# Performance work log

Measured on AMD Instinct MI355X. Metric: run time of the kernel, lower is better.

## Reference

```python
import jax, jax.numpy as jnp
import numpy as np

B, NQ, NC, D, H, HD, FF, RB = 2, 512, 2048, 768, 12, 64, 3072, 64
EPS = 1e-5


def setup_inputs() -> dict:
    key = jax.random.key(0)
    ks = jax.random.split(key, 20)
    def n(k, shape, s=0.02):
        return jax.random.normal(k, shape, jnp.float32) * s
    return dict(
        query_state=n(ks[0], (B, NQ, D), 1.0),
        context_k=n(ks[1], (B, NC, D), 1.0),
        context_v=n(ks[2], (B, NC, D), 1.0),
        query_coords=jax.random.uniform(ks[3], (B, NQ, 2), jnp.float32),
        context_coords=jax.random.uniform(ks[4], (B, NC, 2), jnp.float32),
        sn_g=jnp.ones(D), sn_b=jnp.zeros(D),
        wqkv=n(ks[5], (D, 3 * D)), bqkv=jnp.zeros(3 * D),
        wo_s=n(ks[6], (D, D)), bo_s=jnp.zeros(D),
        cn_g=jnp.ones(D), cn_b=jnp.zeros(D),
        wq=n(ks[7], (D, D)), bq=jnp.zeros(D),
        wk=n(ks[8], (D, D)), bk=jnp.zeros(D),
        wv=n(ks[9], (D, D)), bv=jnp.zeros(D),
        wo_c=n(ks[10], (D, D)), bo_c=jnp.zeros(D),
        rb_w1=n(ks[11], (2, RB), 0.5), rb_b1=jnp.zeros(RB),
        rb_w2=n(ks[12], (RB, H), 0.5), rb_b2=jnp.zeros(H),
        fn_g=jnp.ones(D), fn_b=jnp.zeros(D),
        fw1=n(ks[13], (D, FF)), fb1=jnp.zeros(FF),
        fw2=n(ks[14], (FF, D)), fb2=jnp.zeros(D),
    )


def _ln(x, g, b):
    m = x.mean(-1, keepdims=True)
    v = ((x - m) ** 2).mean(-1, keepdims=True)
    return (x - m) / jnp.sqrt(v + EPS) * g + b


def _heads(x):
    # (B, N, D) -> (B, H, N, HD)
    return x.reshape(x.shape[0], x.shape[1], H, HD).transpose(0, 2, 1, 3)


def reference(query_state, context_k, context_v, query_coords, context_coords,
              sn_g, sn_b, wqkv, bqkv, wo_s, bo_s,
              cn_g, cn_b, wq, bq, wk, bk, wv, bv, wo_c, bo_c,
              rb_w1, rb_b1, rb_w2, rb_b2,
              fn_g, fn_b, fw1, fb1, fw2, fb2):
    scale = HD ** -0.5
    x = query_state

    # ---- pre-norm self-attention (nn.MultiheadAttention equivalent) ----
    qn = _ln(x, sn_g, sn_b)
    qkv = qn @ wqkv + bqkv                      # (B, NQ, 3D)
    q, k, v = jnp.split(qkv, 3, axis=-1)
    q, k, v = _heads(q), _heads(k), _heads(v)   # (B, H, NQ, HD)
    a = jax.nn.softmax(jnp.einsum('bhqd,bhkd->bhqk', q, k) * scale, axis=-1)
    o = jnp.einsum('bhqk,bhkd->bhqd', a, v).transpose(0, 2, 1, 3).reshape(B, NQ, D)
    x = x + o @ wo_s + bo_s

    # ---- relative coordinate bias: MLP(delta) -> (B, H, NQ, NC) ----
    delta = query_coords[:, :, None, :] - context_coords[:, None, :, :]  # (B, NQ, NC, 2)
    bias = jax.nn.gelu(delta @ rb_w1 + rb_b1, approximate=False) @ rb_w2 + rb_b2
    bias = bias.transpose(0, 3, 1, 2)           # (B, H, NQ, NC)

    # ---- pre-norm cross-attention with bias ----
    qn = _ln(x, cn_g, cn_b)
    q = _heads(qn @ wq + bq)                    # (B, H, NQ, HD)
    k = _heads(context_k @ wk + bk)             # (B, H, NC, HD)
    v = _heads(context_v @ wv + bv)
    logits = jnp.einsum('bhqd,bhkd->bhqk', q, k) * scale + bias
    a = jax.nn.softmax(logits, axis=-1)
    o = jnp.einsum('bhqk,bhkd->bhqd', a, v).transpose(0, 2, 1, 3).reshape(B, NQ, D)
    x = x + o @ wo_c + bo_c

    # ---- pre-norm FFN ----
    h = jax.nn.gelu(_ln(x, fn_g, fn_b) @ fw1 + fb1, approximate=False)
    x = x + h @ fw2 + fb2
    return x
```

## Files before the change

kernel.cpp:

```cpp
#include <hip/hip_runtime.h>

#define B_ 2
#define NQ_ 512
#define NC_ 2048
#define D_ 768
#define H_ 12
#define HD_ 64
#define FF_ 3072
#define RB_ 64

typedef unsigned short u16;
typedef __attribute__((ext_vector_type(4))) unsigned short u16x4;
typedef __attribute__((ext_vector_type(8))) short short8;
typedef __attribute__((ext_vector_type(4))) float f32x4;
typedef __attribute__((ext_vector_type(2))) float f32x2;

#define SCL2 0.18033688f

__device__ __forceinline__ float bf2f(u16 u) {
    unsigned int i = ((unsigned int)u) << 16;
    float f; __builtin_memcpy(&f, &i, 4); return f;
}
__device__ __forceinline__ u16 f2bf(float f) {
    unsigned int i; __builtin_memcpy(&i, &f, 4);
    unsigned int r = i + 0x7FFFu + ((i >> 16) & 1u);
    return (u16)(r >> 16);
}
__device__ __forceinline__ float gelu_f(float x) {
    return 0.5f * x * (1.f + erff(x * 0.70710678118654752f));
}
__device__ __forceinline__ float wsum(float v) {
    v += __shfl_xor(v, 32); v += __shfl_xor(v, 16); v += __shfl_xor(v, 8);
    v += __shfl_xor(v, 4);  v += __shfl_xor(v, 2);  v += __shfl_xor(v, 1);
    return v;
}
__device__ __forceinline__ void gload_lds16(const void* g, void* l) {
    __builtin_amdgcn_global_load_lds((const __attribute__((address_space(1))) void*)g,
                                     (__attribute__((address_space(3))) void*)l, 16, 0, 0);
}

__device__ __forceinline__ void wtrans_body(const float* __restrict__ in, u16* __restrict__ out,
                                            int K, int N, int bx, int by, int tid) {
    __shared__ float t[32][33];
    int n0 = bx * 32, k0 = by * 32;
    int tx = tid & 31, ty = tid >> 5;
#pragma unroll
    for (int r = 0; r < 4; ++r)
        t[ty + r * 8][tx] = in[(long)(k0 + ty + r * 8) * N + n0 + tx];
    __syncthreads();
#pragma unroll
    for (int r = 0; r < 4; ++r)
        out[(long)(n0 + ty + r * 8) * K + k0 + tx] = f2bf(t[tx][ty + r * 8]);
}

__global__ __launch_bounds__(256) void wtrans(const float* __restrict__ in, u16* __restrict__ out,
                                              int K, int N) {
    wtrans_body(in, out, K, N, blockIdx.x, blockIdx.y, threadIdx.x);
}

__global__ __launch_bounds__(256) void wtrans5(const float* i0, const float* i1, const float* i2,
                                               const float* i3, const float* i4,
                                               u16* o0, u16* o1, u16* o2, u16* o3, u16* o4) {
    const float* in; u16* out;
    switch (blockIdx.z) {
        case 0: in = i0; out = o0; break;
        case 1: in = i1; out = o1; break;
        case 2: in = i2; out = o2; break;
        case 3: in = i3; out = o3; break;
        default: in = i4; out = o4; break;
    }
    wtrans_body(in, out, 768, 768, blockIdx.x, blockIdx.y, threadIdx.x);
}

__global__ __launch_bounds__(256) void cvtk2(const float* __restrict__ inA, u16* __restrict__ outA,
                                             const float* __restrict__ inB, u16* __restrict__ outB, int n4) {
    int i = blockIdx.x * 256 + threadIdx.x;
    const float* in = blockIdx.y ? inB : inA;
    u16* out = blockIdx.y ? outB : outA;
    if (i < n4) {
        float4 v = ((const float4*)in)[i];
        u16x4 o; o.x = f2bf(v.x); o.y = f2bf(v.y); o.z = f2bf(v.z); o.w = f2bf(v.w);
        ((u16x4*)out)[i] = o;
    }
}

__global__ __launch_bounds__(256) void catbias(const float* __restrict__ a, const float* __restrict__ b,
                                               float* __restrict__ o) {
    int i = blockIdx.x * 256 + threadIdx.x;
    if (i < 768) o[i] = a[i];
    else if (i < 1536) o[i] = b[i - 768];
}

__global__ __launch_bounds__(256) void ln_k(const float* __restrict__ x, const float* __restrict__ g,
                                            const float* __restrict__ bta, u16* __restrict__ out) {
    int row = blockIdx.x, t = threadIdx.x;
    const float* xr = x + (long)row * D_;
    float a0 = xr[t], a1 = xr[t + 256], a2 = xr[t + 512];
    float s = a0 + a1 + a2, s2 = a0 * a0 + a1 * a1 + a2 * a2;
    s = wsum(s); s2 = wsum(s2);
    __shared__ float rb[8];
    int lane = t & 63, wid = t >> 6;
    if (!lane) { rb[wid] = s; rb[wid + 4] = s2; }
    __syncthreads();
    float S = rb[0] + rb[1] + rb[2] + rb[3];
    float S2 = rb[4] + rb[5] + rb[6] + rb[7];
    float mean = S * (1.f / D_);
    float var = S2 * (1.f / D_) - mean * mean;
    float rstd = rsqrtf(var + 1e-5f);
    u16* orow = out + (long)row * D_;
    orow[t]       = f2bf((a0 - mean) * rstd * g[t]       + bta[t]);
    orow[t + 256] = f2bf((a1 - mean) * rstd * g[t + 256] + bta[t + 256]);
    orow[t + 512] = f2bf((a2 - mean) * rstd * g[t + 512] + bta[t + 512]);
}

__global__ __launch_bounds__(256) void bias_mlp7(
    const float* __restrict__ qcoord, const float* __restrict__ ccoord,
    const float* __restrict__ w1, const float* __restrict__ b1,
    const float* __restrict__ w2, const float* __restrict__ b2,
    u16* __restrict__ out) {
    __shared__ float s1[192];
    __shared__ float sw2[RB_ * H_];
    __shared__ float2 sc[256];
    __shared__ u16 sb[12 * 264];
    int tid = threadIdx.x;
    int b = blockIdx.z, q0 = blockIdx.y * 4, c0 = blockIdx.x * 256;
    if (tid < 64) { s1[tid] = w1[tid]; s1[64 + tid] = w1[64 + tid]; s1[128 + tid] = b1[tid]; }
    for (int i = tid; i < RB_ * H_; i += 256) sw2[i] = w2[i];
    sc[tid] = ((const float2*)ccoord)[b * NC_ + c0 + tid];
    __syncthreads();
    int lane = tid & 63, wid = tid >> 6;
    int h = lane & 15, g4 = lane >> 4;
    int j0 = g4 * 8;
    f32x2 wx[8], wy[8], bb[8];
#pragma unroll
    for (int p = 0; p < 4; ++p) {
        wx[p]     = (f32x2){s1[j0 + 2 * p],       s1[j0 + 2 * p + 1]};
        wy[p]     = (f32x2){s1[64 + j0 + 2 * p],  s1[64 + j0 + 2 * p + 1]};
        bb[p]     = (f32x2){s1[128 + j0 + 2 * p], s1[128 + j0 + 2 * p + 1]};
        wx[4 + p] = (f32x2){s1[32 + j0 + 2 * p],  s1[32 + j0 + 2 * p + 1]};
        wy[4 + p] = (f32x2){s1[96 + j0 + 2 * p],  s1[96 + j0 + 2 * p + 1]};
        bb[4 + p] = (f32x2){s1[160 + j0 + 2 * p], s1[160 + j0 + 2 * p + 1]};
    }
    short8 vb0, vb1;
#pragma unroll
    for (int u = 0; u < 8; ++u) {
        vb0[u] = (h < 12) ? (short)f2bf(sw2[(j0 + u) * H_ + h]) : (short)0;
        vb1[u] = (h < 12) ? (short)f2bf(sw2[(32 + j0 + u) * H_ + h]) : (short)0;
    }
    float qx[4], qy[4];
#pragma unroll
    for (int qq = 0; qq < 4; ++qq) {
        qx[qq] = qcoord[(b * NQ_ + q0 + qq) * 2];
        qy[qq] = qcoord[(b * NQ_ + q0 + qq) * 2 + 1];
    }
    float b2v = (h < 12) ? b2[h] : 0.f;
#pragma unroll 1
    for (int qq = 0; qq < 4; ++qq) {
        if (qq) __syncthreads();
#pragma unroll
        for (int it = 0; it < 4; ++it) {
            int ci = wid * 64 + it * 16 + h;
            float2 cc = sc[ci];
            float dx = qx[qq] - cc.x, dy = qy[qq] - cc.y;
            unsigned int pk[8];
#pragma unroll
            for (int p = 0; p < 8; ++p) {
                f32x2 pre = dx * wx[p] + bb[p];
                pre = dy * wy[p] + pre;
                f32x2 xc = __builtin_elementwise_min(
                               __builtin_elementwise_max(pre, (f32x2)(-3.0f)), (f32x2)(3.0f));
                f32x2 u = xc * xc;
                f32x2 v = u * 2.3813e-5f + (-6.8939e-4f);
                v = v * u + 0.0086261f;
                v = v * u + (-0.064949f);
                v = v * u + 0.39837f;
                f32x2 phi = xc * v + 0.5f;
                f32x2 g = pre * phi;
                pk[p] = __builtin_amdgcn_perm(__builtin_bit_cast(unsigned int, g.y),
                                              __builtin_bit_cast(unsigned int, g.x), 0x07060302u);
            }
            uint4 d0 = {pk[0], pk[1], pk[2], pk[3]};
            uint4 d1 = {pk[4], pk[5], pk[6], pk[7]};
            short8 a0 = __builtin_bit_cast(short8, d0);
            short8 a1 = __builtin_bit_cast(short8, d1);
            f32x4 acc = {};
            acc = __builtin_amdgcn_mfma_f32_16x16x32_bf16(a0, vb0, acc, 0, 0, 0);
            acc = __builtin_amdgcn_mfma_f32_16x16x32_bf16(a1, vb1, acc, 0, 0, 0);
            if (h < 12) {
#pragma unroll
                for (int r = 0; r < 4; ++r) {
                    int loc = wid * 64 + it * 16 + g4 * 4 + r;
                    sb[h * 264 + loc] = f2bf((acc[r] + b2v) * 1.4426950f);
                }
            }
        }
        __syncthreads();
        for (int i = tid; i < 12 * 128; i += 256) {
            int row = i >> 7, cp = (i & 127) * 2;
            unsigned int pv = *(const unsigned int*)(sb + row * 264 + cp);
            *(unsigned int*)(out + (((long)(b * H_ + row) * NQ_ + q0 + qq) * NC_ + c0 + cp)) = pv;
        }
    }
}

__global__ __launch_bounds__(256) void vtrans(const u16* __restrict__ in, u16* __restrict__ out,
                                              int NCt, int ldin, int bdiv, long sIb, long sIh) {
    __shared__ u16 t[32][33];
    int z = blockIdx.z, zb = z / bdiv, zh = z % bdiv;
    const u16* ib = in + zb * sIb + zh * sIh;
    int c0 = blockIdx.x * 32, d0 = blockIdx.y * 32;
    int tx = threadIdx.x & 31, ty = threadIdx.x >> 5;
#pragma unroll
    for (int r = 0; r < 4; ++r)
        t[ty + r * 8][tx] = ib[(long)(c0 + ty + r * 8) * ldin + d0 + tx];
    __syncthreads();
#pragma unroll
    for (int r = 0; r < 4; ++r)
        out[(long)z * 64 * NCt + (long)(d0 + ty + r * 8) * NCt + c0 + tx] = t[tx][ty + r * 8];
}

template <int NCT, bool HASBIAS>
__global__ __launch_bounds__(64) void fattn(
    const u16* __restrict__ Qb, const u16* __restrict__ Kb, const u16* __restrict__ Vtb,
    const u16* __restrict__ Bias, u16* __restrict__ Ob, int ldq, int ldk) {
    __shared__ u16 kl[2][128 * 64];
    __shared__ u16 vl[64 * 128];
    __shared__ u16 pl[16 * 128];
    const int lane = threadIdx.x;
    const int h16 = lane & 15, g4 = lane >> 4;
    const int hh = blockIdx.y, b = blockIdx.z, q0 = blockIdx.x * 16;
    const u16* Qrow = Qb + (long)(b * NQ_ + q0 + h16) * ldq + hh * 64;
    short8 qf0 = *(const short8*)(Qrow + g4 * 8);
    short8 qf1 = *(const short8*)(Qrow + 32 + g4 * 8);
    const u16* Kbase = Kb + (long)b * NCT * ldk + hh * 64;
    const u16* Vtbase = Vtb + (long)(b * H_ + hh) * 64 * NCT;

    auto stageK = [&](int buf, int c0) {
#pragma unroll
        for (int i = 0; i < 16; ++i) {
            int ch = i * 64 + lane;
            int row = ch >> 3, col2 = (ch & 7) * 16;
            int scol2 = col2 ^ ((row & 7) << 4);
            gload_lds16(Kbase + (long)(c0 + row) * ldk + (scol2 >> 1), &kl[buf][ch * 8]);
        }
    };
    auto stageV = [&](int c0) {
#pragma unroll
        for (int i = 0; i < 16; ++i) {
            int ch = i * 64 + lane;
            int row = ch >> 4, col2 = (ch & 15) * 16;
            int scol2 = col2 ^ ((row & 15) << 4);
            gload_lds16(Vtbase + (long)row * NCT + c0 + (scol2 >> 1), &vl[ch * 8]);
        }
    };

    float m0[4] = {-1e30f, -1e30f, -1e30f, -1e30f};
    float l0[4] = {0.f, 0.f, 0.f, 0.f};
    f32x4 oacc[4] = {};
    constexpr int T = NCT / 128;
    stageK(0, 0);
    for (int t = 0; t < T; ++t) {
        const int c0 = t * 128, cur = t & 1;
        asm volatile("s_waitcnt lgkmcnt(0)" ::: "memory");
        stageV(c0);
        if (t + 1 < T) stageK(cur ^ 1, c0 + 128);
        if (t + 1 < T) asm volatile("s_waitcnt vmcnt(32)" ::: "memory");
        else           asm volatile("s_waitcnt vmcnt(16)" ::: "memory");
        f32x4 sacc[8] = {};
        const u16* klc = kl[cur];
        __builtin_amdgcn_s_setprio(1);
#pragma unroll
        for (int n = 0; n < 8; ++n) {
            int row = n * 16 + h16, swz = (row & 7) << 4;
#pragma unroll
            for (int ks = 0; ks < 2; ++ks) {
                short8 kf = *(const short8*)((const char*)klc + row * 128 + ((ks * 64 + g4 * 16) ^ swz));
                sacc[n] = __builtin_amdgcn_mfma_f32_16x16x32_bf16(ks ? qf1 : qf0, kf, sacc[n], 0, 0, 0);
            }
        }
        __builtin_amdgcn_s_setprio(0);
        if (t + 1 < T) asm volatile("s_waitcnt vmcnt(16)" ::: "memory");
        else           asm volatile("s_waitcnt vmcnt(0)" ::: "memory");
        float cr[4];
#pragma unroll
        for (int r = 0; r < 4; ++r) {
            float mx = -1e30f;
#pragma unroll
            for (int n = 0; n < 8; ++n) {
                float s = sacc[n][r] * SCL2;
                sacc[n][r] = s; mx = fmaxf(mx, s);
            }
            mx = fmaxf(mx, __shfl_xor(mx, 1)); mx = fmaxf(mx, __shfl_xor(mx, 2));
            mx = fmaxf(mx, __shfl_xor(mx, 4)); mx = fmaxf(mx, __shfl_xor(mx, 8));
            float mn = fmaxf(m0[r], mx);
            cr[r] = __builtin_amdgcn_exp2f(m0[r] - mn); m0[r] = mn;
            float sum = 0.f;
#pragma unroll
            for (int n = 0; n < 8; ++n) {
                float p = __builtin_amdgcn_exp2f(sacc[n][r] - mn); sacc[n][r] = p; sum += p;
            }
            sum += __shfl_xor(sum, 1); sum += __shfl_xor(sum, 2);
            sum += __shfl_xor(sum, 4); sum += __shfl_xor(sum, 8);
            l0[r] = l0[r] * cr[r] + sum;
        }
#pragma unroll
        for (int n = 0; n < 8; ++n)
#pragma unroll
            for (int r = 0; r < 4; ++r) {
                int q = g4 * 4 + r, c = n * 16 + h16;
                *(u16*)((char*)pl + q * 256 + ((c * 2) ^ (q << 4))) =
                    (u16)(__builtin_bit_cast(unsigned int, sacc[n][r]) >> 16);
            }
#pragma unroll
        for (int d = 0; d < 4; ++d) {
            f32x4 o = oacc[d];
            o[0] *= cr[0]; o[1] *= cr[1]; o[2] *= cr[2]; o[3] *= cr[3];
            oacc[d] = o;
        }
        short8 pf[4];
#pragma unroll
        for (int ks = 0; ks < 4; ++ks)
            pf[ks] = *(const short8*)((const char*)pl + h16 * 256 + ((ks * 64 + g4 * 16) ^ (h16 << 4)));
        __builtin_amdgcn_s_setprio(1);
#pragma unroll
        for (int d = 0; d < 4; ++d) {
            int row = d * 16 + h16, swzv = (row & 15) << 4;
#pragma unroll
            for (int ks = 0; ks < 4; ++ks) {
                short8 vf = *(const short8*)((const char*)vl + row * 256 + ((ks * 64 + g4 * 16) ^ swzv));
                oacc[d] = __builtin_amdgcn_mfma_f32_16x16x32_bf16(pf[ks], vf, oacc[d], 0, 0, 0);
            }
        }
        __builtin_amdgcn_s_setprio(0);
    }
    float inv[4];
#pragma unroll
    for (int r = 0; r < 4; ++r) inv[r] = 1.f / l0[r];
    u16* Orow = Ob + (long)(b * NQ_ + q0) * D_ + hh * 64;
#pragma unroll
    for (int d = 0; d < 4; ++d)
#pragma unroll
        for (int r = 0; r < 4; ++r)
            Orow[(long)(g4 * 4 + r) * D_ + d * 16 + h16] = f2bf(oacc[d][r] * inv[r]);
}

template <int T, int S>
__global__ __launch_bounds__(256) void fattn4(
    const u16* __restrict__ Qb, const u16* __restrict__ Kb, const u16* __restrict__ Vtb,
    const u16* __restrict__ Bias, float* __restrict__ Part,
    int ldq, int ldk, int ldv, int NCT) {
    __shared__ u16 kl[2][64 * 64];
    __shared__ u16 vl[64 * 64];
    __shared__ u16 bl[4][16 * 64];
    __shared__ u16 pl[4][16 * 64];
    const int tid = threadIdx.x, lane = tid & 63, wid = tid >> 6;
    const int h16 = lane & 15, g4 = lane >> 4;
    const int qb = blockIdx.x, hh = blockIdx.y;
    const int b = blockIdx.z / S, s = blockIdx.z % S;
    const int q0w = qb * 64 + wid * 16;
    const int cb = s * (T * 64);
    const u16* Qrow = Qb + (long)(b * NQ_ + q0w + h16) * ldq + hh * 64;
    short8 qf0 = *(const short8*)(Qrow + g4 * 8);
    short8 qf1 = *(const short8*)(Qrow + 32 + g4 * 8);
    const u16* Kbase = Kb + (long)b * NCT * ldk + hh * 64;
    const u16* Vtbase = Vtb + (long)(b * H_ + hh) * 64 * ldv;
    const u16* Bbase = Bias + ((long)(b * H_ + hh) * NQ_ + q0w) * NCT;
    u16* mypl = pl[wid];
    const u16* mybl = bl[wid];

    auto stageK = [&](int buf, int c0) {
#pragma unroll
        for (int i = 0; i < 2; ++i) {
            int ch = wid * 128 + i * 64 + lane;
            int row = ch >> 3, col2 = (ch & 7) * 16;
            int scol2 = col2 ^ ((row & 7) << 4);
            gload_lds16(Kbase + (long)(c0 + row) * ldk + (scol2 >> 1), &kl[buf][ch * 8]);
        }
    };
    auto stageV = [&](int c0) {
#pragma unroll
        for (int i = 0; i < 2; ++i) {
            int ch = wid * 128 + i * 64 + lane;
            int row = ch >> 3, col2 = (ch & 7) * 16;
            int scol2 = col2 ^ ((row & 7) << 4);
            gload_lds16(Vtbase + (long)row * ldv + c0 + (scol2 >> 1), &vl[ch * 8]);
        }
    };
    auto stageB = [&](int c0) {
#pragma unroll
        for (int i = 0; i < 2; ++i) {
            int ch = i * 64 + lane;
            int row = ch >> 3, c16 = ch & 7;
            int sc16 = c16 ^ (row & 7);
            gload_lds16(Bbase + (long)row * NCT + c0 + sc16 * 8, &bl[wid][ch * 8]);
        }
    };

    float m0[4] = {-1e30f, -1e30f, -1e30f, -1e30f};
    float l0[4] = {0.f, 0.f, 0.f, 0.f};
    f32x4 oacc[4] = {};
    stageK(0, cb);
    for (int t = 0; t < T; ++t) {
        const int c0 = cb + t * 64, cur = t & 1;
        if (t > 0) {
            asm volatile("s_waitcnt lgkmcnt(0)" ::: "memory");
            __builtin_amdgcn_sched_barrier(0);
            __builtin_amdgcn_s_barrier();
        }
        stageV(c0);
        stageB(c0);
        if (t + 1 < T) stageK(cur ^ 1, c0 + 64);
        if (t + 1 < T) asm volatile("s_waitcnt vmcnt(6)" ::: "memory");
        else           asm volatile("s_waitcnt vmcnt(4)" ::: "memory");
        __builtin_amdgcn_s_barrier();
        f32x4 sacc[4] = {};
        const u16* klc = kl[cur];
        __builtin_amdgcn_s_setprio(1);
#pragma unroll
        for (int n = 0; n < 4; ++n) {
            int row = n * 16 + h16, swz = (row & 7) << 4;
#pragma unroll
            for (int ks = 0; ks < 2; ++ks) {
                short8 kf = *(const short8*)((const char*)klc + row * 128 + ((ks * 64 + g4 * 16) ^ swz));
                sacc[n] = __builtin_amdgcn_mfma_f32_16x16x32_bf16(ks ? qf1 : qf0, kf, sacc[n], 0, 0, 0);
            }
        }
        __builtin_amdgcn_s_setprio(0);
        if (t + 1 < T) asm volatile("s_waitcnt vmcnt(2)" ::: "memory");
        else           asm volatile("s_waitcnt vmcnt(0)" ::: "memory");
        __builtin_amdgcn_s_barrier();
        float cr[4];
#pragma unroll
        for (int r = 0; r < 4; ++r) {
            int q = g4 * 4 + r;
            float mx = -1e30f;
#pragma unroll
            for (int n = 0; n < 4; ++n) {
                float bvv = bf2f(*(const u16*)((const char*)mybl + q * 128 +
                                 (((n * 16 + h16) * 2) ^ ((q & 7) << 4))));
                float sv = sacc[n][r] * SCL2 + bvv;
                sacc[n][r] = sv; mx = fmaxf(mx, sv);
            }
            mx = fmaxf(mx, __shfl_xor(mx, 1)); mx = fmaxf(mx, __shfl_xor(mx, 2));
            mx = fmaxf(mx, __shfl_xor(mx, 4)); mx = fmaxf(mx, __shfl_xor(mx, 8));
            float mn = fmaxf(m0[r], mx);
            cr[r] = __builtin_amdgcn_exp2f(m0[r] - mn); m0[r] = mn;
            float sum = 0.f;
#pragma unroll
            for (int n = 0; n < 4; ++n) {
                float p = __builtin_amdgcn_exp2f(sacc[n][r] - mn); sacc[n][r] = p; sum += p;
            }
            sum += __shfl_xor(sum, 1); sum += __shfl_xor(sum, 2);
            sum += __shfl_xor(sum, 4); sum += __shfl_xor(sum, 8);
            l0[r] = l0[r] * cr[r] + sum;
        }
#pragma unroll
        for (int n = 0; n < 4; ++n)
#pragma unroll
            for (int r = 0; r < 4; ++r) {
                int q = g4 * 4 + r, c = n * 16 + h16;
                *(u16*)((char*)mypl + q * 128 + ((c * 2) ^ ((q & 7) << 4))) =
                    (u16)(__builtin_bit_cast(unsigned int, sacc[n][r]) >> 16);
            }
#pragma unroll
        for (int d = 0; d < 4; ++d) {
            f32x4 o = oacc[d];
            o[0] *= cr[0]; o[1] *= cr[1]; o[2] *= cr[2]; o[3] *= cr[3];
            oacc[d] = o;
        }
        short8 pf[2];
#pragma unroll
        for (int ks = 0; ks < 2; ++ks)
            pf[ks] = *(const short8*)((const char*)mypl + h16 * 128 + ((ks * 64 + g4 * 16) ^ ((h16 & 7) << 4)));
        __builtin_amdgcn_s_setprio(1);
#pragma unroll
        for (int d = 0; d < 4; ++d) {
            int row = d * 16 + h16, swzv = (row & 7) << 4;
#pragma unroll
            for (int ks = 0; ks < 2; ++ks) {
                short8 vf = *(const short8*)((const char*)vl + row * 128 + ((ks * 64 + g4 * 16) ^ swzv));
                oacc[d] = __builtin_amdgcn_mfma_f32_16x16x32_bf16(pf[ks], vf, oacc[d], 0, 0, 0);
            }
        }
        __builtin_amdgcn_s_setprio(0);
    }
    float* P = Part + ((((long)(b * H_ + hh) * 32 + qb * 4 + wid) * S + s) * 1088);
#pragma unroll
    for (int d = 0; d < 4; ++d)
#pragma unroll
        for (int r = 0; r < 4; ++r)
            P[(g4 * 4 + r) * 64 + d * 16 + h16] = oacc[d][r];
    if (h16 == 0) {
#pragma unroll
        for (int r = 0; r < 4; ++r) {
            P[1024 + g4 * 4 + r] = m0[r];
            P[1056 + g4 * 4 + r] = l0[r];
        }
    }
}

__global__ __launch_bounds__(64) void fcomb(const float* __restrict__ Part, u16* __restrict__ Ob) {
    int q16 = blockIdx.x, hh = blockIdx.y, b = blockIdx.z, lane = threadIdx.x;
    const float* base = Part + (((long)(b * H_ + hh) * 32 + q16) * 4) * 1088;
#pragma unroll 4
    for (int q = 0; q < 16; ++q) {
        float m0 = base[1024 + q],        m1 = base[1088 + 1024 + q];
        float m2 = base[2176 + 1024 + q], m3 = base[3264 + 1024 + q];
        float M = fmaxf(fmaxf(m0, m1), fmaxf(m2, m3));
        float w0 = __builtin_amdgcn_exp2f(m0 - M), w1 = __builtin_amdgcn_exp2f(m1 - M);
        float w2 = __builtin_amdgcn_exp2f(m2 - M), w3 = __builtin_amdgcn_exp2f(m3 - M);
        float L = w0 * base[1056 + q] + w1 * base[1088 + 1056 + q] +
                  w2 * base[2176 + 1056 + q] + w3 * base[3264 + 1056 + q];
        float o = w0 * base[q * 64 + lane] + w1 * base[1088 + q * 64 + lane] +
                  w2 * base[2176 + q * 64 + lane] + w3 * base[3264 + q * 64 + lane];
        Ob[(long)(b * NQ_ + q16 * 16 + q) * D_ + hh * 64 + lane] = f2bf(o * (1.f / L));
    }
}

enum { EP_BIAS = 0, EP_SCALE = 1, EP_RES = 3, EP_GELU = 4 };

template <int BM, int BN, int EPI>
__global__ __launch_bounds__(256) void gemm_bt(
    const u16* __restrict__ A, const u16* __restrict__ B, void* __restrict__ Cv,
    const float* __restrict__ bias, const float* __restrict__ res,
    int M, int N, int K, int lda, int ldb, int ldc,
    int bdiv, long sAb, long sAh, long sBb, long sBh, long sCb, long sCh,
    float scale, int biasz) {
    constexpr int BK = 64;
    __shared__ u16 lA[BM * BK];
    __shared__ u16 lB[BN * BK];
    const int z = blockIdx.z;
    const int zb = z / bdiv, zh = z % bdiv;
    const u16* Ab = A + zb * sAb + zh * sAh;
    const u16* Bb = B + zb * sBb + zh * sBh;
    const int bm = blockIdx.y * BM;
    const int bn = blockIdx.x * BN;
    const int tid = threadIdx.x;
    const int lane = tid & 63, wid = tid >> 6;
    const int wm = (wid >> 1) * (BM / 2);
    const int wn = (wid & 1) * (BN / 2);
    constexpr int FM = BM / 32, FN = BN / 32;
    f32x4 acc[FM][FN] = {};
    const int lrow = lane & 15, lk = (lane >> 4) * 8;

    for (int kb = 0; kb < K; kb += BK) {
#pragma unroll
        for (int i = 0; i < (BM * 8) / 256; ++i) {
            int ch = tid + i * 256;
            int r = ch >> 3, c = ch & 7;
            gload_lds16(Ab + (long)(bm + r) * lda + kb + c * 8, lA + ch * 8);
        }
#pragma unroll
        for (int i = 0; i < (BN * 8) / 256; ++i) {
            int ch = tid + i * 256;
            int r = ch >> 3, c = ch & 7;
            gload_lds16(Bb + (long)(bn + r) * ldb + kb + c * 8, lB + ch * 8);
        }
        __syncthreads();
#pragma unroll
        for (int ks = 0; ks < 2; ++ks) {
            short8 af[FM], bfr[FN];
#pragma unroll
            for (int i = 0; i < FM; ++i)
                af[i] = *(const short8*)(lA + (wm + i * 16 + lrow) * BK + ks * 32 + lk);
#pragma unroll
            for (int j = 0; j < FN; ++j)
                bfr[j] = *(const short8*)(lB + (wn + j * 16 + lrow) * BK + ks * 32 + lk);
#pragma unroll
            for (int i = 0; i < FM; ++i)
#pragma unroll
                for (int j = 0; j < FN; ++j)
                    acc[i][j] = __builtin_amdgcn_mfma_f32_16x16x32_bf16(af[i], bfr[j], acc[i][j], 0, 0, 0);
        }
        __syncthreads();
    }

    long coff = zb * sCb + zh * sCh;
#pragma unroll
    for (int i = 0; i < FM; ++i) {
#pragma unroll
        for (int j = 0; j < FN; ++j) {
#pragma unroll
            for (int r = 0; r < 4; ++r) {
                int row = bm + wm + i * 16 + (lane >> 4) * 4 + r;
                int col = bn + wn + j * 16 + (lane & 15);
                long idx = coff + (long)row * ldc + col;
                float v = acc[i][j][r];
                if (EPI == EP_SCALE) {
                    ((u16*)Cv)[idx] = f2bf(v * scale);
                } else if (EPI == EP_RES) {
                    float tt = v + (bias ? bias[col] : 0.f);
                    ((float*)Cv)[idx] = res[idx] + tt;
                } else if (EPI == EP_GELU) {
                    float tt = v + (bias ? bias[col] : 0.f);
                    ((u16*)Cv)[idx] = f2bf(gelu_f(tt));
                } else {
                    float tt = v + (bias ? bias[biasz * zb + col] : 0.f);
                    ((u16*)Cv)[idx] = f2bf(tt);
                }
            }
        }
    }
}

extern "C" void kernel_launch(void* const* d_in, const int* in_sizes, int n_in,
                              void* d_out, int out_size, void* d_ws, size_t ws_size,
                              hipStream_t stream) {
    const float* x_in   = (const float*)d_in[0];
    const float* ctx_k  = (const float*)d_in[1];
    const float* ctx_v  = (const float*)d_in[2];
    const float* qcoord = (const float*)d_in[3];
    const float* ccoord = (const float*)d_in[4];
    const float* sn_g   = (const float*)d_in[5];
    const float* sn_b   = (const float*)d_in[6];
    const float* wqkv   = (const float*)d_in[7];
    const float* bqkv   = (const float*)d_in[8];
    const float* wo_s   = (const float*)d_in[9];
    const float* bo_s   = (const float*)d_in[10];
    const float* cn_g   = (const float*)d_in[11];
    const float* cn_b   = (const float*)d_in[12];
    const float* wq     = (const float*)d_in[13];
    const float* bq     = (const float*)d_in[14];
    const float* wk     = (const float*)d_in[15];
    const float* bk     = (const float*)d_in[16];
    const float* wv     = (const float*)d_in[17];
    const float* bv     = (const float*)d_in[18];
    const float* wo_c   = (const float*)d_in[19];
    const float* bo_c   = (const float*)d_in[20];
    const float* rb_w1  = (const float*)d_in[21];
    const float* rb_b1  = (const float*)d_in[22];
    const float* rb_w2  = (const float*)d_in[23];
    const float* rb_b2  = (const float*)d_in[24];
    const float* fn_g   = (const float*)d_in[25];
    const float* fn_b   = (const float*)d_in[26];
    const float* fw1    = (const float*)d_in[27];
    const float* fb1    = (const float*)d_in[28];
    const float* fw2    = (const float*)d_in[29];
    const float* fb2    = (const float*)d_in[30];

    char* ws = (char*)d_ws;
    size_t off = 0;
    auto alloc = [&](size_t bytes) -> void* {
        void* p = ws + off; off += (bytes + 255) & ~(size_t)255; return p;
    };
    u16* wT_qkv = (u16*)alloc((size_t)2304 * 768 * 2);
    u16* wT_os  = (u16*)alloc((size_t)768 * 768 * 2);
    u16* wT_q   = (u16*)alloc((size_t)768 * 768 * 2);
    u16* wT_k   = (u16*)alloc((size_t)768 * 768 * 2);
    u16* wT_v   = (u16*)alloc((size_t)768 * 768 * 2);
    u16* wT_oc  = (u16*)alloc((size_t)768 * 768 * 2);
    u16* wT_f1  = (u16*)alloc((size_t)3072 * 768 * 2);
    u16* wT_f2  = (u16*)alloc((size_t)768 * 3072 * 2);
    u16* ckb    = (u16*)alloc((size_t)B_ * NC_ * D_ * 2);
    u16* cvb    = (u16*)alloc((size_t)B_ * NC_ * D_ * 2);
    u16* xln    = (u16*)alloc((size_t)1024 * 768 * 2);
    u16* qkv    = (u16*)alloc((size_t)1024 * 2304 * 2);
    u16* vts    = (u16*)alloc((size_t)24 * 64 * 512 * 2);
    u16* oatt   = (u16*)alloc((size_t)1024 * 768 * 2);
    float* x1   = (float*)alloc((size_t)1024 * 768 * 4);
    u16* xln2   = (u16*)alloc((size_t)1024 * 768 * 2);
    u16* qc     = (u16*)alloc((size_t)1024 * 768 * 2);
    u16* kc     = (u16*)alloc((size_t)4096 * 768 * 2);
    u16* vc     = (u16*)alloc((size_t)4096 * 768 * 2);
    u16* clog   = (u16*)alloc((size_t)24 * 512 * 2048 * 2);
    u16* vtc    = (u16*)alloc((size_t)24 * 64 * 2048 * 2);
    u16* oc2    = (u16*)alloc((size_t)1024 * 768 * 2);
    float* x2   = (float*)alloc((size_t)1024 * 768 * 4);
    u16* xln3   = (u16*)alloc((size_t)1024 * 768 * 2);
    u16* ffh    = (u16*)alloc((size_t)1024 * 3072 * 2);
    float* part = (float*)alloc((size_t)2 * H_ * 32 * 4 * 1088 * 4);
    float* bkv  = (float*)alloc((size_t)1536 * 4);
    (void)ws_size; (void)in_sizes; (void)n_in; (void)out_size;

    wtrans<<<dim3(2304 / 32, 768 / 32), 256, 0, stream>>>(wqkv, wT_qkv, 768, 2304);
    wtrans5<<<dim3(24, 24, 5), 256, 0, stream>>>(wo_s, wq, wk, wv, wo_c,
                                                 wT_os, wT_q, wT_k, wT_v, wT_oc);
    wtrans<<<dim3(3072 / 32, 768 / 32), 256, 0, stream>>>(fw1, wT_f1, 768, 3072);
    wtrans<<<dim3(768 / 32, 3072 / 32), 256, 0, stream>>>(fw2, wT_f2, 3072, 768);
    cvtk2<<<dim3(B_ * NC_ * D_ / 4 / 256, 2), 256, 0, stream>>>(ctx_k, ckb, ctx_v, cvb, B_ * NC_ * D_ / 4);
    catbias<<<6, 256, 0, stream>>>(bk, bv, bkv);

    ln_k<<<1024, 256, 0, stream>>>(x_in, sn_g, sn_b, xln);
    gemm_bt<64, 128, EP_BIAS><<<dim3(2304 / 128, 1024 / 64, 1), 256, 0, stream>>>(
        xln, wT_qkv, qkv, bqkv, nullptr, 1024, 2304, 768, 768, 768, 2304,
        1, 0, 0, 0, 0, 0, 0, 1.f, 0);
    bias_mlp7<<<dim3(NC_ / 256, NQ_ / 4, B_), 256, 0, stream>>>(qcoord, ccoord, rb_w1, rb_b1, rb_w2, rb_b2, clog);
    vtrans<<<dim3(512 / 32, 2, 24), 256, 0, stream>>>(qkv + 1536, vts, 512, 2304, 12, (long)512 * 2304, 64);
    fattn<512, false><<<dim3(NQ_ / 16, H_, B_), 64, 0, stream>>>(
        qkv, qkv + 768, vts, nullptr, oatt, 2304, 2304);
    gemm_bt<32, 64, EP_RES><<<dim3(768 / 64, 1024 / 32, 1), 256, 0, stream>>>(
        oatt, wT_os, x1, bo_s, x_in, 1024, 768, 768, 768, 768, 768,
        1, 0, 0, 0, 0, 0, 0, 1.f, 0);

    ln_k<<<1024, 256, 0, stream>>>(x1, cn_g, cn_b, xln2);
    gemm_bt<32, 64, EP_BIAS><<<dim3(768 / 64, 1024 / 32, 1), 256, 0, stream>>>(
        xln2, wT_q, qc, bq, nullptr, 1024, 768, 768, 768, 768, 768,
        1, 0, 0, 0, 0, 0, 0, 1.f, 0);
    gemm_bt<64, 128, EP_BIAS><<<dim3(768 / 128, 4096 / 64, 2), 256, 0, stream>>>(
        ckb, wT_k, kc, bkv, nullptr, 4096, 768, 768, 768, 768, 768,
        1, (long)B_ * NC_ * D_, 0, (long)768 * 768, 0, (long)4096 * 768, 0, 1.f, 768);
    vtrans<<<dim3(2048 / 32, 2, 24), 256, 0, stream>>>(vc, vtc, 2048, 768, 12, (long)2048 * 768, 64);
    fattn4<8, 4><<<dim3(8, H_, B_ * 4), 256, 0, stream>>>(
        qc, kc, vtc, clog, part, 768, 768, 2048, 2048);
    fcomb<<<dim3(32, H_, B_), 64, 0, stream>>>(part, oc2);
    gemm_bt<32, 64, EP_RES><<<dim3(768 / 64, 1024 / 32, 1), 256, 0, stream>>>(
        oc2, wT_oc, x2, bo_c, x1, 1024, 768, 768, 768, 768, 768,
        1, 0, 0, 0, 0, 0, 0, 1.f, 0);

    ln_k<<<1024, 256, 0, stream>>>(x2, fn_g, fn_b, xln3);
    gemm_bt<64, 128, EP_GELU><<<dim3(3072 / 128, 1024 / 64, 1), 256, 0, stream>>>(
        xln3, wT_f1, ffh, fb1, nullptr, 1024, 3072, 768, 768, 768, 3072,
        1, 0, 0, 0, 0, 0, 0, 1.f, 0);
    gemm_bt<32, 64, EP_RES><<<dim3(768 / 64, 1024 / 32, 1), 256, 0, stream>>>(
        ffh, wT_f2, (float*)d_out, fb2, x2, 1024, 768, 3072, 3072, 3072, 768,
        1, 0, 0, 0, 0, 0, 0, 1.f, 0);
}
```

Before: 256.0 us.

## Merge prep kernels into one launch and co-schedule KV projection with bias MLP

Replaces the six weight-transpose, convert and bias-concat launches with a single flat-indexed prep kernel. It also moves the relative-bias MLP out of the main sequence into a combined kernel whose first 768 blocks do the K/V projection GEMM and whose remaining blocks compute the bias. The aim is to cut launch overhead and let the two independent workloads fill the GPU together. In exchange the shared-memory footprint is the union of both paths, which may lower occupancy, and block ordering decides how well the two parts overlap.

Measured after the change: 242.0 us. 1.06x faster.

```diff
diff --git a/kernel.cpp b/kernel.cpp
--- a/kernel.cpp
+++ b/kernel.cpp
@@ -53,42 +53,50 @@
         out[(long)(n0 + ty + r * 8) * K + k0 + tx] = f2bf(t[tx][ty + r * 8]);
 }
 
-__global__ __launch_bounds__(256) void wtrans(const float* __restrict__ in, u16* __restrict__ out,
-                                              int K, int N) {
-    wtrans_body(in, out, K, N, blockIdx.x, blockIdx.y, threadIdx.x);
-}
-
-__global__ __launch_bounds__(256) void wtrans5(const float* i0, const float* i1, const float* i2,
-                                               const float* i3, const float* i4,
-                                               u16* o0, u16* o1, u16* o2, u16* o3, u16* o4) {
-    const float* in; u16* out;
-    switch (blockIdx.z) {
-        case 0: in = i0; out = o0; break;
-        case 1: in = i1; out = o1; break;
-        case 2: in = i2; out = o2; break;
-        case 3: in = i3; out = o3; break;
-        default: in = i4; out = o4; break;
-    }
-    wtrans_body(in, out, 768, 768, blockIdx.x, blockIdx.y, threadIdx.x);
-}
-
-__global__ __launch_bounds__(256) void cvtk2(const float* __restrict__ inA, u16* __restrict__ outA,
-                                             const float* __restrict__ inB, u16* __restrict__ outB, int n4) {
-    int i = blockIdx.x * 256 + threadIdx.x;
-    const float* in = blockIdx.y ? inB : inA;
-    u16* out = blockIdx.y ? outB : outA;
-    if (i < n4) {
-        float4 v = ((const float4*)in)[i];
+__global__ __launch_bounds__(256) void prep(
+    const float* wqkv, u16* wT_qkv,
+    const float* wo_s, const float* wq, const float* wk, const float* wv, const float* wo_c,
+    u16* wT_os, u16* wT_q, u16* wT_k, u16* wT_v, u16* wT_oc,
+    const float* fw1, u16* wT_f1, const float* fw2, u16* wT_f2,
+    const float* ctx_k, u16* ckb, const float* ctx_v, u16* cvb,
+    const float* bk, const float* bv, float* bkv) {
+    int i = blockIdx.x, tid = threadIdx.x;
+    if (i < 1728) { wtrans_body(wqkv, wT_qkv, 768, 2304, i % 72, i / 72, tid); return; }
+    i -= 1728;
+    if (i < 2880) {
+        int z = i / 576, rem = i % 576;
+        const float* in; u16* out;
+        switch (z) {
+            case 0: in = wo_s; out = wT_os; break;
+            case 1: in = wq;   out = wT_q;  break;
+            case 2: in = wk;   out = wT_k;  break;
+            case 3: in = wv;   out = wT_v;  break;
+            default: in = wo_c; out = wT_oc; break;
+        }
+        wtrans_body(in, out, 768, 768, rem % 24, rem / 24, tid);
+        return;
+    }
+    i -= 2880;
+    if (i < 2304) { wtrans_body(fw1, wT_f1, 768, 3072, i % 96, i / 96, tid); return; }
+    i -= 2304;
+    if (i < 2304) { wtrans_body(fw2, wT_f2, 3072, 768, i % 24, i / 24, tid); return; }
+    i -= 2304;
+    if (i < 6144) {
+        int y = i / 3072;
+        int ii = (i % 3072) * 256 + tid;
+        const float* in = y ? ctx_v : ctx_k;
+        u16* out = y ? cvb : ckb;
+        float4 v = ((const float4*)in)[ii];
         u16x4 o; o.x = f2bf(v.x); o.y = f2bf(v.y); o.z = f2bf(v.z); o.w = f2bf(v.w);
-        ((u16x4*)out)[i] = o;
-    }
-}
-
-__global__ __launch_bounds__(256) void catbias(const float* __restrict__ a, const float* __restrict__ b,
-                                               float* __restrict__ o) {
-    int i = blockIdx.x * 256 + threadIdx.x;
-    if (i < 768) o[i] = a[i];
-    else if (i < 1536) o[i] = b[i - 768];
+        ((u16x4*)out)[ii] = o;
+        return;
+    }
+    i -= 6144;
+    {
+        int j = i * 256 + tid;
+        if (j < 768) bkv[j] = bk[j];
+        else if (j < 1536) bkv[j] = bv[j - 768];
+    }
 }
 
 __global__ __launch_bounds__(256) void ln_k(const float* __restrict__ x, const float* __restrict__ g,
@@ -113,17 +121,17 @@
     orow[t + 512] = f2bf((a2 - mean) * rstd * g[t + 512] + bta[t + 512]);
 }
 
-__global__ __launch_bounds__(256) void bias_mlp7(
+#define BIAS_SMEM_BYTES (5888 + 12 * 264 * 2)
+__device__ __forceinline__ void bias_body(char* smem,
     const float* __restrict__ qcoord, const float* __restrict__ ccoord,
     const float* __restrict__ w1, const float* __restrict__ b1,
     const float* __restrict__ w2, const float* __restrict__ b2,
-    u16* __restrict__ out) {
-    __shared__ float s1[192];
-    __shared__ float sw2[RB_ * H_];
-    __shared__ float2 sc[256];
-    __shared__ u16 sb[12 * 264];
-    int tid = threadIdx.x;
-    int b = blockIdx.z, q0 = blockIdx.y * 4, c0 = blockIdx.x * 256;
+    u16* __restrict__ out, int cx, int q4, int b, int tid) {
+    float* s1 = (float*)smem;
+    float* sw2 = (float*)(smem + 768);
+    float2* sc = (float2*)(smem + 3840);
+    u16* sb = (u16*)(smem + 5888);
+    int q0 = q4 * 4, c0 = cx * 256;
     if (tid < 64) { s1[tid] = w1[tid]; s1[64 + tid] = w1[64 + tid]; s1[128 + tid] = b1[tid]; }
     for (int i = tid; i < RB_ * H_; i += 256) sw2[i] = w2[i];
     sc[tid] = ((const float2*)ccoord)[b * NC_ + c0 + tid];
@@ -520,22 +528,19 @@
 enum { EP_BIAS = 0, EP_SCALE = 1, EP_RES = 3, EP_GELU = 4 };
 
 template <int BM, int BN, int EPI>
-__global__ __launch_bounds__(256) void gemm_bt(
+__device__ __forceinline__ void gemm_body(
+    u16* lA, u16* lB,
     const u16* __restrict__ A, const u16* __restrict__ B, void* __restrict__ Cv,
     const float* __restrict__ bias, const float* __restrict__ res,
     int M, int N, int K, int lda, int ldb, int ldc,
     int bdiv, long sAb, long sAh, long sBb, long sBh, long sCb, long sCh,
-    float scale, int biasz) {
+    float scale, int biasz, int bx, int by, int z, int tid) {
     constexpr int BK = 64;
-    __shared__ u16 lA[BM * BK];
-    __shared__ u16 lB[BN * BK];
-    const int z = blockIdx.z;
     const int zb = z / bdiv, zh = z % bdiv;
     const u16* Ab = A + zb * sAb + zh * sAh;
     const u16* Bb = B + zb * sBb + zh * sBh;
-    const int bm = blockIdx.y * BM;
-    const int bn = blockIdx.x * BN;
-    const int tid = threadIdx.x;
+    const int bm = by * BM;
+    const int bn = bx * BN;
     const int lane = tid & 63, wid = tid >> 6;
     const int wm = (wid >> 1) * (BM / 2);
     const int wn = (wid & 1) * (BN / 2);
@@ -600,6 +605,43 @@
                 }
             }
         }
+    }
+}
+
+template <int BM, int BN, int EPI>
+__global__ __launch_bounds__(256) void gemm_bt(
+    const u16* __restrict__ A, const u16* __restrict__ B, void* __restrict__ Cv,
+    const float* __restrict__ bias, const float* __restrict__ res,
+    int M, int N, int K, int lda, int ldb, int ldc,
+    int bdiv, long sAb, long sAh, long sBb, long sBh, long sCb, long sCh,
+    float scale, int biasz) {
+    __shared__ u16 lA[BM * 64];
+    __shared__ u16 lB[BN * 64];
+    gemm_body<BM, BN, EPI>(lA, lB, A, B, Cv, bias, res, M, N, K, lda, ldb, ldc,
+                           bdiv, sAb, sAh, sBb, sBh, sCb, sCh, scale, biasz,
+                           blockIdx.x, blockIdx.y, blockIdx.z, threadIdx.x);
+}
+
+__global__ __launch_bounds__(256) void kvproj_bias(
+    const u16* __restrict__ ckb, const u16* __restrict__ wT_k, u16* __restrict__ kc,
+    const float* __restrict__ bkv,
+    const float* __restrict__ qcoord, const float* __restrict__ ccoord,
+    const float* __restrict__ rb_w1, const float* __restrict__ rb_b1,
+    const float* __restrict__ rb_w2, const float* __restrict__ rb_b2,
+    u16* __restrict__ clog) {
+    __shared__ __attribute__((aligned(16))) char smem[(64 + 128) * 64 * 2];
+    int idx = blockIdx.x, tid = threadIdx.x;
+    if (idx < 768) {
+        int z = idx / 384, rem = idx % 384;
+        int bx = rem % 6, by = rem / 6;
+        gemm_body<64, 128, EP_BIAS>((u16*)smem, (u16*)(smem + 64 * 64 * 2),
+            ckb, wT_k, kc, bkv, nullptr, 4096, 768, 768, 768, 768, 768,
+            1, (long)B_ * NC_ * D_, 0, (long)768 * 768, 0, (long)4096 * 768, 0,
+            1.f, 768, bx, by, z, tid);
+    } else {
+        int bidx = idx - 768;
+        int cx = bidx & 7, q4 = (bidx >> 3) & 127, b = bidx >> 10;
+        bias_body(smem, qcoord, ccoord, rb_w1, rb_b1, rb_w2, rb_b2, clog, cx, q4, b, tid);
     }
 }
 
@@ -672,19 +714,15 @@
     float* bkv  = (float*)alloc((size_t)1536 * 4);
     (void)ws_size; (void)in_sizes; (void)n_in; (void)out_size;
 
-    wtrans<<<dim3(2304 / 32, 768 / 32), 256, 0, stream>>>(wqkv, wT_qkv, 768, 2304);
-    wtrans5<<<dim3(24, 24, 5), 256, 0, stream>>>(wo_s, wq, wk, wv, wo_c,
-                                                 wT_os, wT_q, wT_k, wT_v, wT_oc);
-    wtrans<<<dim3(3072 / 32, 768 / 32), 256, 0, stream>>>(fw1, wT_f1, 768, 3072);
-    wtrans<<<dim3(768 / 32, 3072 / 32), 256, 0, stream>>>(fw2, wT_f2, 3072, 768);
-    cvtk2<<<dim3(B_ * NC_ * D_ / 4 / 256, 2), 256, 0, stream>>>(ctx_k, ckb, ctx_v, cvb, B_ * NC_ * D_ / 4);
-    catbias<<<6, 256, 0, stream>>>(bk, bv, bkv);
+    prep<<<15366, 256, 0, stream>>>(wqkv, wT_qkv, wo_s, wq, wk, wv, wo_c,
+                                    wT_os, wT_q, wT_k, wT_v, wT_oc,
+                                    fw1, wT_f1, fw2, wT_f2,
+                                    ctx_k, ckb, ctx_v, cvb, bk, bv, bkv);
 
     ln_k<<<1024, 256, 0, stream>>>(x_in, sn_g, sn_b, xln);
     gemm_bt<64, 128, EP_BIAS><<<dim3(2304 / 128, 1024 / 64, 1), 256, 0, stream>>>(
         xln, wT_qkv, qkv, bqkv, nullptr, 1024, 2304, 768, 768, 768, 2304,
         1, 0, 0, 0, 0, 0, 0, 1.f, 0);
-    bias_mlp7<<<dim3(NC_ / 256, NQ_ / 4, B_), 256, 0, stream>>>(qcoord, ccoord, rb_w1, rb_b1, rb_w2, rb_b2, clog);
     vtrans<<<dim3(512 / 32, 2, 24), 256, 0, stream>>>(qkv + 1536, vts, 512, 2304, 12, (long)512 * 2304, 64);
     fattn<512, false><<<dim3(NQ_ / 16, H_, B_), 64, 0, stream>>>(
         qkv, qkv + 768, vts, nullptr, oatt, 2304, 2304);
@@ -696,9 +734,8 @@
     gemm_bt<32, 64, EP_BIAS><<<dim3(768 / 64, 1024 / 32, 1), 256, 0, stream>>>(
         xln2, wT_q, qc, bq, nullptr, 1024, 768, 768, 768, 768, 768,
         1, 0, 0, 0, 0, 0, 0, 1.f, 0);
-    gemm_bt<64, 128, EP_BIAS><<<dim3(768 / 128, 4096 / 64, 2), 256, 0, stream>>>(
-        ckb, wT_k, kc, bkv, nullptr, 4096, 768, 768, 768, 768, 768,
-        1, (long)B_ * NC_ * D_, 0, (long)768 * 768, 0, (long)4096 * 768, 0, 1.f, 768);
+    kvproj_bias<<<2816, 256, 0, stream>>>(ckb, wT_k, kc, bkv,
+                                          qcoord, ccoord, rb_w1, rb_b1, rb_w2, rb_b2, clog);
     vtrans<<<dim3(2048 / 32, 2, 24), 256, 0, stream>>>(vc, vtc, 2048, 768, 12, (long)2048 * 768, 64);
     fattn4<8, 4><<<dim3(8, H_, B_ * 4), 256, 0, stream>>>(
         qc, kc, vtc, clog, part, 768, 768, 2048, 2048);
```
